# Optimization experiments

Measured on AMD Instinct MI355X. Metric: run time of the kernel, lower is better.

## Reference

```python
import jax, jax.numpy as jnp
import numpy as np

C_IN = 128      # in_channels == num_hiddens (required for residual add)
C_RES = 64      # num_residual_hiddens
D = 512         # representation_dim (in == out)


def _complete_conv1d(x, W, Wc, bc):
    """Faithful fused form of CompleteConv1d.forward for batch=1.

    x:  (1, C, D)   input
    W:  (C, D, D)   stacked per-channel Linear weights (W[c] maps D->D)
    Wc: (OC, C)     1x1 Conv1d weight (kernel dim squeezed)
    bc: (OC,)       1x1 Conv1d bias

    The autograd jacobian of the per-channel linear map is block diagonal:
      xy_grad[c, o, c', i] = W[c, o, i] * delta(c, c')
    so xy_grad_reduced[o, i] = sum_c W[c, o, i], node[i] = argmax_o of that,
    and the python double loop is a scatter-add:
      (y - y_neg)[0, f, n] = sum_{i : node[i]==n} W[f, n, i] * x[0, f, i]
    (y itself, including the Linear biases, cancels exactly).
    """
    d = W.shape[1]
    node = jnp.argmax(jnp.sum(W, axis=0), axis=0)          # (D,) argmax over o
    idx = jnp.arange(d)
    vals = W[:, node, idx] * x[0]                           # (C, D): W[f,node[i],i]*x[0,f,i]
    diff = jnp.zeros_like(x[0]).at[:, node].add(vals)       # scatter-add over repeated nodes
    out = jnp.einsum('oc,cd->od', Wc, diff) + bc[:, None]   # 1x1 conv == channel GEMM
    return out[None]                                        # (1, OC, D)


def setup_inputs() -> dict:
    key = jax.random.key(0)
    ks = jax.random.split(key, 7)
    s = lambda k, shape, scale: (jax.random.normal(k, shape, dtype=jnp.float32) * scale)
    return {
        'x':   s(ks[0], (1, C_IN, D), 1.0),
        'W1':  s(ks[1], (C_IN, D, D), D ** -0.5),
        'Wc1': s(ks[2], (C_RES, C_IN), C_IN ** -0.5),
        'bc1': s(ks[3], (C_RES,), 0.02),
        'W2':  s(ks[4], (C_RES, D, D), D ** -0.5),
        'Wc2': s(ks[5], (C_IN, C_RES), C_RES ** -0.5),
        'bc2': s(ks[6], (C_IN,), 0.02),
    }


def reference(x, W1, Wc1, bc1, W2, Wc2, bc2):
    # nn.ReLU(True) inside the Sequential mutates x in place, so the residual
    # add uses relu(x), not x.
    xr = jax.nn.relu(x)
    h1 = _complete_conv1d(xr, W1, Wc1, bc1)
    h2 = _complete_conv1d(jax.nn.relu(h1), W2, Wc2, bc2)
    return xr + h2
```

## Files before the change

kernel.cpp:

```cpp
#include <hip/hip_runtime.h>

#define C_IN  128
#define C_RES 64
#define D     512
#define DD    (D * D)
#define U4    (DD / 4)

__device__ inline void acc4(float4& a, const float4& w) {
    a.x += w.x; a.y += w.y; a.z += w.z; a.w += w.w;
}

__device__ inline void sum8(float4& a, const float4* __restrict__ p, int stride) {
    float4 r0 = p[0 * (size_t)stride];
    float4 r1 = p[1 * (size_t)stride];
    float4 r2 = p[2 * (size_t)stride];
    float4 r3 = p[3 * (size_t)stride];
    float4 r4 = p[4 * (size_t)stride];
    float4 r5 = p[5 * (size_t)stride];
    float4 r6 = p[6 * (size_t)stride];
    float4 r7 = p[7 * (size_t)stride];
    acc4(a, r0); acc4(a, r1); acc4(a, r2); acc4(a, r3);
    acc4(a, r4); acc4(a, r5); acc4(a, r6); acc4(a, r7);
}

__global__ void __launch_bounds__(256, 4)
sum_kernel(const float* __restrict__ W1, const float* __restrict__ W2,
           float* __restrict__ P1, float* __restrict__ P2,
           float* __restrict__ diff_zero) {
    const int gtid = blockIdx.x * 256 + threadIdx.x;
    const int u = gtid & (U4 - 1);
    const int p = gtid >> 16;

    const float4* w1p = (const float4*)W1 + (size_t)(32 * p) * U4 + u;
    float4 a1 = make_float4(0.f, 0.f, 0.f, 0.f);
    sum8(a1, w1p + (size_t)0  * U4, U4);
    sum8(a1, w1p + (size_t)8  * U4, U4);
    sum8(a1, w1p + (size_t)16 * U4, U4);
    sum8(a1, w1p + (size_t)24 * U4, U4);
    ((float4*)P1)[p * U4 + u] = a1;

    const float4* w2p = (const float4*)W2 + (size_t)(16 * p) * U4 + u;
    float4 a2 = make_float4(0.f, 0.f, 0.f, 0.f);
    sum8(a2, w2p + (size_t)0 * U4, U4);
    sum8(a2, w2p + (size_t)8 * U4, U4);
    ((float4*)P2)[p * U4 + u] = a2;

    if (gtid < (C_IN + C_RES) * D)
        diff_zero[gtid] = 0.f;
}

__global__ void argmax_scatter_kernel(const float* __restrict__ P1,
                                      const float* __restrict__ P2,
                                      const float* __restrict__ W1,
                                      const float* __restrict__ W2,
                                      const float* __restrict__ x,
                                      float* __restrict__ diff1,
                                      float* __restrict__ w2v,
                                      int* __restrict__ node2) {
    __shared__ float lv[256];
    __shared__ int   li[256];
    __shared__ int   node_s[8];

    const int  tid = threadIdx.x;
    const int  bid = blockIdx.x;
    const bool st1 = bid < 64;
    const int  i0  = (st1 ? bid : bid - 64) * 8;
    const float* __restrict__ P = st1 ? P1 : P2;

    const int il = tid & 7;
    const int ol = tid >> 3;
    float best = -__builtin_inff();
    int   bidx = D;
    for (int k = 0; k < 16; ++k) {
        int o = ol + (k << 5);
        int base = o * D + i0 + il;
        float v = P[base] + P[DD + base] + P[2 * DD + base] + P[3 * DD + base];
        if (v > best) { best = v; bidx = o; }
    }
    lv[tid] = best; li[tid] = bidx;
    __syncthreads();
    for (int s = 128; s >= 8; s >>= 1) {
        if (tid < s) {
            float v2 = lv[tid + s]; int i2 = li[tid + s];
            if (v2 > lv[tid] || (v2 == lv[tid] && i2 < li[tid])) {
                lv[tid] = v2; li[tid] = i2;
            }
        }
        __syncthreads();
    }
    if (tid < 8) {
        node_s[tid] = li[tid];
        if (!st1) node2[i0 + tid] = li[tid];
    }
    __syncthreads();

    if (st1) {
        for (int idx = tid; idx < C_IN * 8; idx += 256) {
            int ii = idx & 7;
            int c  = idx >> 3;
            int i  = i0 + ii;
            int n  = node_s[ii];
            float xv = fmaxf(x[c * D + i], 0.f);
            float w  = W1[(size_t)c * DD + (size_t)n * D + i];
            atomicAdd(&diff1[c * D + n], w * xv);
        }
    } else {
        for (int idx = tid; idx < C_RES * 8; idx += 256) {
            int ii = idx & 7;
            int c  = idx >> 3;
            int i  = i0 + ii;
            int n  = node_s[ii];
            w2v[c * D + i] = W2[(size_t)c * DD + (size_t)n * D + i];
        }
    }
}

__global__ void conv1_scatter2_kernel(const float* __restrict__ Wc1,
                                      const float* __restrict__ bc1,
                                      const float* __restrict__ diff1,
                                      const float* __restrict__ w2v,
                                      const int* __restrict__ node2,
                                      float* __restrict__ diff2) {
    __shared__ float wc[C_IN];
    const int c = blockIdx.x >> 1;
    const int i = ((blockIdx.x & 1) << 8) + threadIdx.x;
    if (threadIdx.x < C_IN) wc[threadIdx.x] = Wc1[c * C_IN + threadIdx.x];
    __syncthreads();

    float acc = bc1[c];
#pragma unroll 8
    for (int cc = 0; cc < C_IN; ++cc)
        acc += wc[cc] * diff1[cc * D + i];
    float x2 = fmaxf(acc, 0.f);
    int n = node2[i];
    atomicAdd(&diff2[c * D + n], w2v[c * D + i] * x2);
}

__global__ void final_kernel(const float* __restrict__ Wc2,
                             const float* __restrict__ bc2,
                             const float* __restrict__ diff2,
                             const float* __restrict__ x,
                             float* __restrict__ out) {
    __shared__ float wc[C_RES];
    const int o = blockIdx.x >> 1;
    const int d = ((blockIdx.x & 1) << 8) + threadIdx.x;
    if (threadIdx.x < C_RES) wc[threadIdx.x] = Wc2[o * C_RES + threadIdx.x];
    __syncthreads();

    float acc = bc2[o];
#pragma unroll 8
    for (int c = 0; c < C_RES; ++c)
        acc += wc[c] * diff2[c * D + d];
    out[o * D + d] = acc + fmaxf(x[o * D + d], 0.f);
}

extern "C" void kernel_launch(void* const* d_in, const int* in_sizes, int n_in,
                              void* d_out, int out_size, void* d_ws, size_t ws_size,
                              hipStream_t stream) {
    const float* x   = (const float*)d_in[0];
    const float* W1  = (const float*)d_in[1];
    const float* Wc1 = (const float*)d_in[2];
    const float* bc1 = (const float*)d_in[3];
    const float* W2  = (const float*)d_in[4];
    const float* Wc2 = (const float*)d_in[5];
    const float* bc2 = (const float*)d_in[6];
    float* out = (float*)d_out;

    float* ws    = (float*)d_ws;
    float* P1    = ws;
    float* P2    = P1 + 4 * DD;
    float* diff1 = P2 + 4 * DD;
    float* diff2 = diff1 + C_IN * D;
    float* w2v   = diff2 + C_RES * D;
    int*   node2 = (int*)(w2v + C_RES * D);

    sum_kernel<<<1024, 256, 0, stream>>>(W1, W2, P1, P2, diff1);
    argmax_scatter_kernel<<<128, 256, 0, stream>>>(P1, P2, W1, W2, x,
                                                   diff1, w2v, node2);
    conv1_scatter2_kernel<<<128, 256, 0, stream>>>(Wc1, bc1, diff1, w2v,
                                                   node2, diff2);
    final_kernel<<<256, 256, 0, stream>>>(Wc2, bc2, diff2, x, out);
}
```

Baseline: 269.2 us.

## Fuse argmax, conv1 and final stages into one cooperative kernel with grid syncs

Merges the argmax/scatter, first 1x1 conv plus second scatter, and final conv stages into a single cooperative kernel separated by grid-wide syncs, cutting two kernel launches. The argmax stage now uses 256 blocks of 4 columns each instead of 128 blocks of 8, to spread the work across more blocks. This trades launch overhead for the cost of grid.sync barriers and the cooperative launch path.

```diff
diff --git a/kernel.cpp b/kernel.cpp
--- a/kernel.cpp
+++ b/kernel.cpp
@@ -1,4 +1,7 @@
 #include <hip/hip_runtime.h>
+#include <hip/hip_cooperative_groups.h>
+
+namespace cg = cooperative_groups;
 
 #define C_IN  128
 #define C_RES 64
@@ -49,109 +52,111 @@
         diff_zero[gtid] = 0.f;
 }
 
-__global__ void argmax_scatter_kernel(const float* __restrict__ P1,
-                                      const float* __restrict__ P2,
-                                      const float* __restrict__ W1,
-                                      const float* __restrict__ W2,
-                                      const float* __restrict__ x,
-                                      float* __restrict__ diff1,
-                                      float* __restrict__ w2v,
-                                      int* __restrict__ node2) {
+__global__ void __launch_bounds__(256)
+tail_kernel(const float* __restrict__ P1,  const float* __restrict__ P2,
+            const float* __restrict__ W1,  const float* __restrict__ W2,
+            const float* __restrict__ Wc1, const float* __restrict__ bc1,
+            const float* __restrict__ Wc2, const float* __restrict__ bc2,
+            const float* __restrict__ x,
+            float* __restrict__ diff1,
+            float* __restrict__ w2v, int* __restrict__ node2,
+            float* __restrict__ out) {
+    cg::grid_group grid = cg::this_grid();
+    const int tid = threadIdx.x;
+    const int bid = blockIdx.x;
+
     __shared__ float lv[256];
     __shared__ int   li[256];
-    __shared__ int   node_s[8];
+    __shared__ int   node_s[4];
+    __shared__ float wc[C_IN];
 
-    const int  tid = threadIdx.x;
-    const int  bid = blockIdx.x;
-    const bool st1 = bid < 64;
-    const int  i0  = (st1 ? bid : bid - 64) * 8;
-    const float* __restrict__ P = st1 ? P1 : P2;
+    float* __restrict__ diff2 = diff1 + C_IN * D;
 
-    const int il = tid & 7;
-    const int ol = tid >> 3;
-    float best = -__builtin_inff();
-    int   bidx = D;
-    for (int k = 0; k < 16; ++k) {
-        int o = ol + (k << 5);
-        int base = o * D + i0 + il;
-        float v = P[base] + P[DD + base] + P[2 * DD + base] + P[3 * DD + base];
-        if (v > best) { best = v; bidx = o; }
-    }
-    lv[tid] = best; li[tid] = bidx;
-    __syncthreads();
-    for (int s = 128; s >= 8; s >>= 1) {
-        if (tid < s) {
-            float v2 = lv[tid + s]; int i2 = li[tid + s];
-            if (v2 > lv[tid] || (v2 == lv[tid] && i2 < li[tid])) {
-                lv[tid] = v2; li[tid] = i2;
+    {
+        const bool st1 = bid < 128;
+        const int  i0  = (st1 ? bid : bid - 128) * 4;
+        const float* __restrict__ P = st1 ? P1 : P2;
+
+        const int il = tid & 3;
+        const int ol = tid >> 2;
+        float best = -__builtin_inff();
+        int   bidx = D;
+        for (int k = 0; k < 8; ++k) {
+            int o = ol + (k << 6);
+            int base = o * D + i0 + il;
+            float v = P[base] + P[DD + base] + P[2 * DD + base] + P[3 * DD + base];
+            if (v > best) { best = v; bidx = o; }
+        }
+        lv[tid] = best; li[tid] = bidx;
+        __syncthreads();
+        for (int s = 128; s >= 4; s >>= 1) {
+            if (tid < s) {
+                float v2 = lv[tid + s]; int i2 = li[tid + s];
+                if (v2 > lv[tid] || (v2 == lv[tid] && i2 < li[tid])) {
+                    lv[tid] = v2; li[tid] = i2;
+                }
+            }
+            __syncthreads();
+        }
+        if (tid < 4) {
+            node_s[tid] = li[tid];
+            if (!st1) node2[i0 + tid] = li[tid];
+        }
+        __syncthreads();
+
+        if (st1) {
+            for (int idx = tid; idx < C_IN * 4; idx += 256) {
+                int ii = idx & 3;
+                int c  = idx >> 2;
+                int i  = i0 + ii;
+                int n  = node_s[ii];
+                float xv = fmaxf(x[c * D + i], 0.f);
+                float w  = W1[(size_t)c * DD + (size_t)n * D + i];
+                atomicAdd(&diff1[c * D + n], w * xv);
+            }
+        } else {
+            int ii = tid & 3;
+            int c  = tid >> 2;
+            if (c < C_RES) {
+                int i = i0 + ii;
+                int n = node_s[ii];
+                w2v[c * D + i] = W2[(size_t)c * DD + (size_t)n * D + i];
             }
         }
+    }
+
+    grid.sync();
+
+    if (bid < 128) {
+        const int c = bid >> 1;
+        const int i = ((bid & 1) << 8) + tid;
+        if (tid < C_IN) wc[tid] = Wc1[c * C_IN + tid];
         __syncthreads();
+
+        float acc = bc1[c];
+#pragma unroll 8
+        for (int cc = 0; cc < C_IN; ++cc)
+            acc += wc[cc] * diff1[cc * D + i];
+        float x2 = fmaxf(acc, 0.f);
+        int n = node2[i];
+        atomicAdd(&diff2[c * D + n], w2v[c * D + i] * x2);
     }
-    if (tid < 8) {
-        node_s[tid] = li[tid];
-        if (!st1) node2[i0 + tid] = li[tid];
+
+    grid.sync();
+
+    {
+        const int o = bid >> 1;
+        const int d = ((bid & 1) << 8) + tid;
+        __syncthreads();
+        if (tid < C_RES) wc[tid] = Wc2[o * C_RES + tid];
+        __syncthreads();
+
+        float acc = bc2[o];
+#pragma unroll 8
+        for (int c = 0; c < C_RES; ++c)
+            acc += wc[c] * diff2[c * D + d];
+        out[o * D + d] = acc + fmaxf(x[o * D + d], 0.f);
     }
-    __syncthreads();
-
-    if (st1) {
-        for (int idx = tid; idx < C_IN * 8; idx += 256) {
-            int ii = idx & 7;
-            int c  = idx >> 3;
-            int i  = i0 + ii;
-            int n  = node_s[ii];
-            float xv = fmaxf(x[c * D + i], 0.f);
-            float w  = W1[(size_t)c * DD + (size_t)n * D + i];
-            atomicAdd(&diff1[c * D + n], w * xv);
-        }
-    } else {
-        for (int idx = tid; idx < C_RES * 8; idx += 256) {
-            int ii = idx & 7;
-            int c  = idx >> 3;
-            int i  = i0 + ii;
-            int n  = node_s[ii];
-            w2v[c * D + i] = W2[(size_t)c * DD + (size_t)n * D + i];
-        }
-    }
-}
-
-__global__ void conv1_scatter2_kernel(const float* __restrict__ Wc1,
-                                      const float* __restrict__ bc1,
-                                      const float* __restrict__ diff1,
-                                      const float* __restrict__ w2v,
-                                      const int* __restrict__ node2,
-                                      float* __restrict__ diff2) {
-    __shared__ float wc[C_IN];
-    const int c = blockIdx.x >> 1;
-    const int i = ((blockIdx.x & 1) << 8) + threadIdx.x;
-    if (threadIdx.x < C_IN) wc[threadIdx.x] = Wc1[c * C_IN + threadIdx.x];
-    __syncthreads();
-
-    float acc = bc1[c];
-#pragma unroll 8
-    for (int cc = 0; cc < C_IN; ++cc)
-        acc += wc[cc] * diff1[cc * D + i];
-    float x2 = fmaxf(acc, 0.f);
-    int n = node2[i];
-    atomicAdd(&diff2[c * D + n], w2v[c * D + i] * x2);
-}
-
-__global__ void final_kernel(const float* __restrict__ Wc2,
-                             const float* __restrict__ bc2,
-                             const float* __restrict__ diff2,
-                             const float* __restrict__ x,
-                             float* __restrict__ out) {
-    __shared__ float wc[C_RES];
-    const int o = blockIdx.x >> 1;
-    const int d = ((blockIdx.x & 1) << 8) + threadIdx.x;
-    if (threadIdx.x < C_RES) wc[threadIdx.x] = Wc2[o * C_RES + threadIdx.x];
-    __syncthreads();
-
-    float acc = bc2[o];
-#pragma unroll 8
-    for (int c = 0; c < C_RES; ++c)
-        acc += wc[c] * diff2[c * D + d];
-    out[o * D + d] = acc + fmaxf(x[o * D + d], 0.f);
 }
 
 extern "C" void kernel_launch(void* const* d_in, const int* in_sizes, int n_in,
@@ -170,14 +175,16 @@
     float* P1    = ws;
     float* P2    = P1 + 4 * DD;
     float* diff1 = P2 + 4 * DD;
-    float* diff2 = diff1 + C_IN * D;
-    float* w2v   = diff2 + C_RES * D;
+    float* w2v   = diff1 + (C_IN + C_RES) * D;
     int*   node2 = (int*)(w2v + C_RES * D);
 
     sum_kernel<<<1024, 256, 0, stream>>>(W1, W2, P1, P2, diff1);
-    argmax_scatter_kernel<<<128, 256, 0, stream>>>(P1, P2, W1, W2, x,
-                                                   diff1, w2v, node2);
-    conv1_scatter2_kernel<<<128, 256, 0, stream>>>(Wc1, bc1, diff1, w2v,
-                                                   node2, diff2);
-    final_kernel<<<256, 256, 0, stream>>>(Wc2, bc2, diff2, x, out);
+
+    void* args[] = {
+        (void*)&P1, (void*)&P2, (void*)&W1, (void*)&W2, (void*)&Wc1,
+        (void*)&bc1, (void*)&Wc2, (void*)&bc2, (void*)&x, (void*)&diff1,
+        (void*)&w2v, (void*)&node2, (void*)&out,
+    };
+    hipLaunchCooperativeKernel((void*)tail_kernel, dim3(256), dim3(256),
+                               args, 0, stream);
 }
```

Result: slower. 348.8 us (+29.6%).

## Reduce channel sums fully in sum_kernel, dropping partial-sum buffers

Applied to the files above, without the earlier changes.

The channel-sum reduction is restructured so each block owns one output row and reduces all channels, with the two half-blocks combining through shared memory. It writes a single summed matrix per weight instead of four partial sums. The argmax kernel then reads one value per element instead of four. The W1 and W2 work is now split unevenly across blocks (512 blocks sum 64 channels each, 512 sum 32), which may unbalance the load. Each thread also runs a longer serial chain of strided loads.

```diff
diff --git a/kernel.cpp b/kernel.cpp
--- a/kernel.cpp
+++ b/kernel.cpp
@@ -10,47 +10,74 @@
     a.x += w.x; a.y += w.y; a.z += w.z; a.w += w.w;
 }
 
-__device__ inline void sum8(float4& a, const float4* __restrict__ p, int stride) {
-    float4 r0 = p[0 * (size_t)stride];
-    float4 r1 = p[1 * (size_t)stride];
-    float4 r2 = p[2 * (size_t)stride];
-    float4 r3 = p[3 * (size_t)stride];
-    float4 r4 = p[4 * (size_t)stride];
-    float4 r5 = p[5 * (size_t)stride];
-    float4 r6 = p[6 * (size_t)stride];
-    float4 r7 = p[7 * (size_t)stride];
+__device__ inline void sum8(float4& a, const float4* __restrict__ p, size_t stride) {
+    float4 r0 = p[0 * stride];
+    float4 r1 = p[1 * stride];
+    float4 r2 = p[2 * stride];
+    float4 r3 = p[3 * stride];
+    float4 r4 = p[4 * stride];
+    float4 r5 = p[5 * stride];
+    float4 r6 = p[6 * stride];
+    float4 r7 = p[7 * stride];
     acc4(a, r0); acc4(a, r1); acc4(a, r2); acc4(a, r3);
     acc4(a, r4); acc4(a, r5); acc4(a, r6); acc4(a, r7);
 }
 
 __global__ void __launch_bounds__(256, 4)
 sum_kernel(const float* __restrict__ W1, const float* __restrict__ W2,
-           float* __restrict__ P1, float* __restrict__ P2,
+           float* __restrict__ S1, float* __restrict__ S2,
            float* __restrict__ diff_zero) {
-    const int gtid = blockIdx.x * 256 + threadIdx.x;
-    const int u = gtid & (U4 - 1);
-    const int p = gtid >> 16;
-
-    const float4* w1p = (const float4*)W1 + (size_t)(32 * p) * U4 + u;
-    float4 a1 = make_float4(0.f, 0.f, 0.f, 0.f);
-    sum8(a1, w1p + (size_t)0  * U4, U4);
-    sum8(a1, w1p + (size_t)8  * U4, U4);
-    sum8(a1, w1p + (size_t)16 * U4, U4);
-    sum8(a1, w1p + (size_t)24 * U4, U4);
-    ((float4*)P1)[p * U4 + u] = a1;
-
-    const float4* w2p = (const float4*)W2 + (size_t)(16 * p) * U4 + u;
-    float4 a2 = make_float4(0.f, 0.f, 0.f, 0.f);
-    sum8(a2, w2p + (size_t)0 * U4, U4);
-    sum8(a2, w2p + (size_t)8 * U4, U4);
-    ((float4*)P2)[p * U4 + u] = a2;
-
+    const int tid = threadIdx.x;
+    const int bid = blockIdx.x;
+    const int i4  = tid & 127;
+    const int ch  = tid >> 7;
+    const size_t st = 2 * (size_t)U4;
+
+    __shared__ float4 sh[128];
+
+    if (bid < 512) {
+        const int o = bid;
+        const float4* p = (const float4*)W1 + (size_t)ch * U4
+                        + (size_t)o * (D / 4) + i4;
+        float4 a = make_float4(0.f, 0.f, 0.f, 0.f);
+        sum8(a, p + 0  * st, st);
+        sum8(a, p + 8  * st, st);
+        sum8(a, p + 16 * st, st);
+        sum8(a, p + 24 * st, st);
+        sum8(a, p + 32 * st, st);
+        sum8(a, p + 40 * st, st);
+        sum8(a, p + 48 * st, st);
+        sum8(a, p + 56 * st, st);
+        if (ch) sh[i4] = a;
+        __syncthreads();
+        if (!ch) {
+            acc4(a, sh[i4]);
+            ((float4*)S1)[o * (D / 4) + i4] = a;
+        }
+    } else {
+        const int o = bid - 512;
+        const float4* p = (const float4*)W2 + (size_t)ch * U4
+                        + (size_t)o * (D / 4) + i4;
+        float4 a = make_float4(0.f, 0.f, 0.f, 0.f);
+        sum8(a, p + 0  * st, st);
+        sum8(a, p + 8  * st, st);
+        sum8(a, p + 16 * st, st);
+        sum8(a, p + 24 * st, st);
+        if (ch) sh[i4] = a;
+        __syncthreads();
+        if (!ch) {
+            acc4(a, sh[i4]);
+            ((float4*)S2)[o * (D / 4) + i4] = a;
+        }
+    }
+
+    const int gtid = bid * 256 + tid;
     if (gtid < (C_IN + C_RES) * D)
         diff_zero[gtid] = 0.f;
 }
 
-__global__ void argmax_scatter_kernel(const float* __restrict__ P1,
-                                      const float* __restrict__ P2,
+__global__ void argmax_scatter_kernel(const float* __restrict__ S1,
+                                      const float* __restrict__ S2,
                                       const float* __restrict__ W1,
                                       const float* __restrict__ W2,
                                       const float* __restrict__ x,
@@ -65,7 +92,7 @@
     const int  bid = blockIdx.x;
     const bool st1 = bid < 64;
     const int  i0  = (st1 ? bid : bid - 64) * 8;
-    const float* __restrict__ P = st1 ? P1 : P2;
+    const float* __restrict__ S = st1 ? S1 : S2;
 
     const int il = tid & 7;
     const int ol = tid >> 3;
@@ -73,8 +100,7 @@
     int   bidx = D;
     for (int k = 0; k < 16; ++k) {
         int o = ol + (k << 5);
-        int base = o * D + i0 + il;
-        float v = P[base] + P[DD + base] + P[2 * DD + base] + P[3 * DD + base];
+        float v = S[o * D + i0 + il];
         if (v > best) { best = v; bidx = o; }
     }
     lv[tid] = best; li[tid] = bidx;
@@ -167,15 +193,15 @@
     float* out = (float*)d_out;
 
     float* ws    = (float*)d_ws;
-    float* P1    = ws;
-    float* P2    = P1 + 4 * DD;
-    float* diff1 = P2 + 4 * DD;
+    float* S1    = ws;
+    float* S2    = S1 + DD;
+    float* diff1 = S2 + DD;
     float* diff2 = diff1 + C_IN * D;
     float* w2v   = diff2 + C_RES * D;
     int*   node2 = (int*)(w2v + C_RES * D);
 
-    sum_kernel<<<1024, 256, 0, stream>>>(W1, W2, P1, P2, diff1);
-    argmax_scatter_kernel<<<128, 256, 0, stream>>>(P1, P2, W1, W2, x,
+    sum_kernel<<<1024, 256, 0, stream>>>(W1, W2, S1, S2, diff1);
+    argmax_scatter_kernel<<<128, 256, 0, stream>>>(S1, S2, W1, W2, x,
                                                    diff1, w2v, node2);
     conv1_scatter2_kernel<<<128, 256, 0, stream>>>(Wc1, bc1, diff1, w2v,
                                                    node2, diff2);
```

Result: faster. 263.0 us (-2.3%).
